# Optimization experiments

Measured on AMD Instinct MI355X. Metric: run time of the kernel, lower is better.

The kernel has to match this reference:

```python
import jax, jax.numpy as jnp
import numpy as np

EPS = 1e-5
GROUPS = 32


def group_norm(x, w, b):
    # x: [N, C]; GroupNorm over 1x1 spatial == per-group norm over C//GROUPS chans
    N, C = x.shape
    xg = x.reshape(N, GROUPS, C // GROUPS)
    mu = xg.mean(-1, keepdims=True)
    var = xg.var(-1, keepdims=True)
    xn = ((xg - mu) * jax.lax.rsqrt(var + EPS)).reshape(N, C)
    return xn * w + b


def rb(x, gn1w, gn1b, c1w, c1b, gn2w, gn2b, c2w, c2b):
    # Conv2d 3x3 pad=1 on a 1x1 spatial input: only the center tap sees data
    # (all other taps hit zero padding), so it reduces exactly to a GEMM with
    # the [out, in] center slice of the kernel.
    h = jax.nn.silu(group_norm(x, gn1w, gn1b))
    h = h @ c1w[:, :, 1, 1].T + c1b
    h = jax.nn.silu(group_norm(h, gn2w, gn2b))
    h = h @ c2w[:, :, 1, 1].T + c2b
    return h + x  # skip == Identity (in_ch == out_ch)


def setup_inputs() -> dict:
    key = jax.random.key(0)
    ks = jax.random.split(key, 20)
    BS, CAND, D, H, W = 32, 2048, 256, 32, 32
    s = 0.05
    inp = {
        "gimage": jax.random.normal(ks[0], (BS, D, H, W), dtype=jnp.float32),
        "pts": jax.random.randint(ks[1], (BS, CAND, 1, 2), 0, 256, dtype=jnp.int32),
        # two stacked RB blocks
        "gn1_w": jnp.ones((2, D), jnp.float32),
        "gn1_b": jnp.zeros((2, D), jnp.float32),
        "conv1_w": jax.random.normal(ks[2], (2, D, D, 3, 3), jnp.float32) * s,
        "conv1_b": jnp.zeros((2, D), jnp.float32),
        "gn2_w": jnp.ones((2, D), jnp.float32),
        "gn2_b": jnp.zeros((2, D), jnp.float32),
        "conv2_w": jax.random.normal(ks[3], (2, D, D, 3, 3), jnp.float32) * s,
        "conv2_b": jnp.zeros((2, D), jnp.float32),
        # class_embed: Linear(256, 2)
        "cls_w": jax.random.normal(ks[4], (2, D), jnp.float32) * s,
        "cls_b": jnp.zeros((2,), jnp.float32),
        # bbox_embed: MLP(256, 256, 4, 3)
        "mlp_w1": jax.random.normal(ks[5], (D, D), jnp.float32) * s,
        "mlp_b1": jnp.zeros((D,), jnp.float32),
        "mlp_w2": jax.random.normal(ks[6], (D, D), jnp.float32) * s,
        "mlp_b2": jnp.zeros((D,), jnp.float32),
        "mlp_w3": jax.random.normal(ks[7], (4, D), jnp.float32) * s,
        "mlp_b3": jnp.zeros((4,), jnp.float32),
    }
    return inp


def reference(gimage, pts, gn1_w, gn1_b, conv1_w, conv1_b, gn2_w, gn2_b,
              conv2_w, conv2_b, cls_w, cls_b, mlp_w1, mlp_b1, mlp_w2, mlp_b2,
              mlp_w3, mlp_b3):
    bs, C, H, W = gimage.shape
    c = pts.shape[1]
    # patch_idx = (pts // 8)[:, :, 0, :] -> (iy, ix) per (batch, candidate)
    idx = pts[:, :, 0, :] // 8                      # [bs, c, 2]
    lin = idx[..., 0] * W + idx[..., 1]             # [bs, c] flat spatial index
    g = gimage.reshape(bs, C, H * W)
    feat = jnp.take_along_axis(g, lin[:, None, :].astype(jnp.int32), axis=2)  # [bs, C, c]
    x = feat.transpose(0, 2, 1).reshape(bs * c, C)  # [(bs c), 256]

    for i in range(2):  # convLayer = Sequential(RB, RB)
        x = rb(x, gn1_w[i], gn1_b[i], conv1_w[i], conv1_b[i],
               gn2_w[i], gn2_b[i], conv2_w[i], conv2_b[i])

    logits = x @ cls_w.T + cls_b                    # [(bs c), 2]
    h = jax.nn.relu(x @ mlp_w1.T + mlp_b1)
    h = jax.nn.relu(h @ mlp_w2.T + mlp_b2)
    boxes = jax.nn.sigmoid(h @ mlp_w3.T + mlp_b3)   # [(bs c), 4]

    pred_logits = logits.reshape(bs, c, 2)
    pred_boxes = boxes.reshape(bs, c, 4)
    return pred_logits, pred_boxes
```

## Files before the change

kernel.cpp:

```cpp
#include <hip/hip_runtime.h>


typedef __attribute__((ext_vector_type(8))) _Float16 half8;
typedef __attribute__((ext_vector_type(4))) float f32x4;

#define AS 264

#define NHALF  393216
#define OFF_WC1 0
#define OFF_WC2 131072
#define OFF_W1  262144
#define OFF_W2  327680
#define WS_NEED 1572864

__device__ __forceinline__ float sigm(float y) { return 1.f / (1.f + __expf(-y)); }

template <int CTRL>
__device__ __forceinline__ float dppadd(float v) {
  union { float f; int i; } u, r;
  u.f = v;
  r.i = __builtin_amdgcn_update_dpp(0, u.i, CTRL, 0xf, 0xf, true);
  return v + r.f;
}
#define DPP_X1 0xB1
#define DPP_X2 0x4E
#define DPP_X7 0x141
#define DPP_XF 0x140

__device__ __forceinline__ float gsum8(float v) {
  v = dppadd<DPP_X1>(v);
  v = dppadd<DPP_X2>(v);
  v = dppadd<DPP_X7>(v);
  return v;
}
__device__ __forceinline__ float gsum16(float v) {
  v = dppadd<DPP_X1>(v);
  v = dppadd<DPP_X2>(v);
  v = dppadd<DPP_X7>(v);
  v = dppadd<DPP_XF>(v);
  return v;
}

__global__ __launch_bounds__(256) void prep(const float* __restrict__ c1w,
                                            const float* __restrict__ c2w,
                                            const float* __restrict__ w1,
                                            const float* __restrict__ w2,
                                            _Float16* __restrict__ ws) {
  int i = blockIdx.x * 256 + threadIdx.x;
  {
    float v = c1w[(size_t)i * 9 + 4];
    _Float16 h = (_Float16)v;
    ws[OFF_WC1 + i] = h;
    ws[NHALF + OFF_WC1 + i] = (_Float16)(v - (float)h);
  }
  {
    float v = c2w[(size_t)i * 9 + 4];
    _Float16 h = (_Float16)v;
    ws[OFF_WC2 + i] = h;
    ws[NHALF + OFF_WC2 + i] = (_Float16)(v - (float)h);
  }
  if (i < 65536) {
    float v = w1[i];
    _Float16 h = (_Float16)v;
    ws[OFF_W1 + i] = h;
    ws[NHALF + OFF_W1 + i] = (_Float16)(v - (float)h);
    v = w2[i];
    h = (_Float16)v;
    ws[OFF_W2 + i] = h;
    ws[NHALF + OFF_W2 + i] = (_Float16)(v - (float)h);
  }
}

__device__ __forceinline__ void hl_store(_Float16* __restrict__ Ah,
                                         _Float16* __restrict__ Al,
                                         int idx, float v) {
  _Float16 h = (_Float16)v;
  Ah[idx] = h;
  Al[idx] = (_Float16)(v - (float)h);
}

struct BF { half8 h[4], l[4]; };

template <int KT>
__device__ __forceinline__ void loadB(BF& B,
    const _Float16* __restrict__ Wh, const _Float16* __restrict__ Wl,
    size_t boff) {
  #pragma unroll
  for (int nt = 0; nt < 4; nt++) {
    B.h[nt] = *(const half8*)(Wh + boff + (nt << 12) + KT * 32);
    B.l[nt] = *(const half8*)(Wl + boff + (nt << 12) + KT * 32);
  }
}

template <int KT>
__device__ __forceinline__ void computeKt(f32x4 acc[2][4],
    const _Float16* __restrict__ Ah, const _Float16* __restrict__ Al,
    int aoff, const BF& B) {
  half8 ah0 = *(const half8*)(Ah + aoff + KT * 32);
  half8 ah1 = *(const half8*)(Ah + aoff + 16 * AS + KT * 32);
  half8 al0 = *(const half8*)(Al + aoff + KT * 32);
  half8 al1 = *(const half8*)(Al + aoff + 16 * AS + KT * 32);
  #pragma unroll
  for (int nt = 0; nt < 4; nt++)
    acc[0][nt] = __builtin_amdgcn_mfma_f32_16x16x32_f16(ah0, B.h[nt], acc[0][nt], 0, 0, 0);
  #pragma unroll
  for (int nt = 0; nt < 4; nt++)
    acc[1][nt] = __builtin_amdgcn_mfma_f32_16x16x32_f16(ah1, B.h[nt], acc[1][nt], 0, 0, 0);
  #pragma unroll
  for (int nt = 0; nt < 4; nt++)
    acc[0][nt] = __builtin_amdgcn_mfma_f32_16x16x32_f16(ah0, B.l[nt], acc[0][nt], 0, 0, 0);
  #pragma unroll
  for (int nt = 0; nt < 4; nt++)
    acc[1][nt] = __builtin_amdgcn_mfma_f32_16x16x32_f16(ah1, B.l[nt], acc[1][nt], 0, 0, 0);
  #pragma unroll
  for (int nt = 0; nt < 4; nt++)
    acc[0][nt] = __builtin_amdgcn_mfma_f32_16x16x32_f16(al0, B.h[nt], acc[0][nt], 0, 0, 0);
  #pragma unroll
  for (int nt = 0; nt < 4; nt++)
    acc[1][nt] = __builtin_amdgcn_mfma_f32_16x16x32_f16(al1, B.h[nt], acc[1][nt], 0, 0, 0);
}

__device__ __forceinline__ void mfma_body(f32x4 acc[2][4], BF& B0,
    const _Float16* __restrict__ Ah, const _Float16* __restrict__ Al,
    const _Float16* __restrict__ Wh, const _Float16* __restrict__ Wl,
    int aoff, size_t boff) {
  BF B1;
  #pragma unroll
  for (int mt = 0; mt < 2; mt++)
    #pragma unroll
    for (int nt = 0; nt < 4; nt++)
      acc[mt][nt] = (f32x4){0.f, 0.f, 0.f, 0.f};
  __syncthreads();
  loadB<1>(B1, Wh, Wl, boff);
  computeKt<0>(acc, Ah, Al, aoff, B0);
  loadB<2>(B0, Wh, Wl, boff);
  computeKt<1>(acc, Ah, Al, aoff, B1);
  loadB<3>(B1, Wh, Wl, boff);
  computeKt<2>(acc, Ah, Al, aoff, B0);
  loadB<4>(B0, Wh, Wl, boff);
  computeKt<3>(acc, Ah, Al, aoff, B1);
  loadB<5>(B1, Wh, Wl, boff);
  computeKt<4>(acc, Ah, Al, aoff, B0);
  loadB<6>(B0, Wh, Wl, boff);
  computeKt<5>(acc, Ah, Al, aoff, B1);
  loadB<7>(B1, Wh, Wl, boff);
  computeKt<6>(acc, Ah, Al, aoff, B0);
  computeKt<7>(acc, Ah, Al, aoff, B1);
}

__device__ __forceinline__ void gn_x_to_A(const float x[2][4][4],
    const float* __restrict__ gnw, const float* __restrict__ gnb,
    int col, int quad, int nb,
    _Float16* __restrict__ Ah, _Float16* __restrict__ Al) {
  #pragma unroll
  for (int nt = 0; nt < 4; nt++) {
    int n = nb + (nt << 4) + col;
    float gwv = gnw[n], gbv = gnb[n];
    #pragma unroll
    for (int mt = 0; mt < 2; mt++) {
      #pragma unroll
      for (int rg = 0; rg < 4; rg++) {
        float v = x[mt][nt][rg];
        float s = gsum8(v);
        float q = gsum8(v * v);
        float mu = s * 0.125f;
        float rs = rsqrtf(q * 0.125f - mu * mu + 1e-5f);
        float y = (v - mu) * rs * gwv + gbv;
        float sv = y * sigm(y);
        hl_store(Ah, Al, ((mt << 4) + (quad << 2) + rg) * AS + n, sv);
      }
    }
  }
}

__device__ __forceinline__ void epi_gn_to_A(const f32x4 acc[2][4],
    const float* __restrict__ bias,
    const float* __restrict__ gnw, const float* __restrict__ gnb,
    int col, int quad, int nb,
    _Float16* __restrict__ Ah, _Float16* __restrict__ Al) {
  #pragma unroll
  for (int nt = 0; nt < 4; nt++) {
    int n = nb + (nt << 4) + col;
    float bv = bias[n];
    float gwv = gnw[n], gbv = gnb[n];
    #pragma unroll
    for (int mt = 0; mt < 2; mt++) {
      #pragma unroll
      for (int rg = 0; rg < 4; rg++) {
        float v = acc[mt][nt][rg] + bv;
        float s = gsum8(v);
        float q = gsum8(v * v);
        float mu = s * 0.125f;
        float rs = rsqrtf(q * 0.125f - mu * mu + 1e-5f);
        float y = (v - mu) * rs * gwv + gbv;
        float sv = y * sigm(y);
        hl_store(Ah, Al, ((mt << 4) + (quad << 2) + rg) * AS + n, sv);
      }
    }
  }
}

__device__ __forceinline__ void epi_relu_to_A(const f32x4 acc[2][4],
    const float* __restrict__ bias, int col, int quad, int nb,
    _Float16* __restrict__ Ah, _Float16* __restrict__ Al) {
  #pragma unroll
  for (int nt = 0; nt < 4; nt++) {
    int n = nb + (nt << 4) + col;
    float bv = bias[n];
    #pragma unroll
    for (int mt = 0; mt < 2; mt++)
      #pragma unroll
      for (int rg = 0; rg < 4; rg++)
        hl_store(Ah, Al, ((mt << 4) + (quad << 2) + rg) * AS + n,
                 fmaxf(acc[mt][nt][rg] + bv, 0.f));
  }
}

__global__ __launch_bounds__(256, 3) void fused_mfma(
    const float* __restrict__ gimage, const int* __restrict__ pts,
    const float* __restrict__ gn1w, const float* __restrict__ gn1b,
    const float* __restrict__ c1b,
    const float* __restrict__ gn2w, const float* __restrict__ gn2b,
    const float* __restrict__ c2b,
    const float* __restrict__ clsw, const float* __restrict__ clsb,
    const float* __restrict__ b1, const float* __restrict__ b2,
    const float* __restrict__ w3, const float* __restrict__ b3,
    const _Float16* __restrict__ ws, float* __restrict__ out) {
  __shared__ _Float16 Ah[32 * AS];
  __shared__ _Float16 Al[32 * AS];
  __shared__ float red[4][32][4];

  const int t = threadIdx.x;
  const int w = t >> 6;
  const int lane = t & 63;
  const int col = lane & 15;
  const int quad = lane >> 4;
  const int nb = w << 6;
  const int bsw = ((blockIdx.x & 7) << 8) | (blockIdx.x >> 3);
  const int row0 = bsw << 5;
  const int rbase = quad << 2;

  const int aoff = col * AS + (quad << 3);
  const size_t boff = (((size_t)(nb + col)) << 8) + (quad << 3);
  const _Float16* wsl = ws + NHALF;

  float x[2][4][4];
  {
    int lin[2][4];
    #pragma unroll
    for (int mt = 0; mt < 2; mt++)
      #pragma unroll
      for (int rg = 0; rg < 4; rg++) {
        int grow = row0 + (mt << 4) + rbase + rg;
        int p0 = pts[2 * grow], p1 = pts[2 * grow + 1];
        lin[mt][rg] = ((p0 >> 3) << 5) + (p1 >> 3);
      }
    const float* gbase = gimage + (((size_t)((row0 >> 11) << 8)) << 10);
    #pragma unroll
    for (int nt = 0; nt < 4; nt++) {
      const float* gc = gbase + (((size_t)(nb + (nt << 4) + col)) << 10);
      #pragma unroll
      for (int mt = 0; mt < 2; mt++)
        #pragma unroll
        for (int rg = 0; rg < 4; rg++)
          x[mt][nt][rg] = gc[lin[mt][rg]];
    }
  }

  f32x4 acc[2][4];
  BF B0;

  loadB<0>(B0, ws + OFF_WC1, wsl + OFF_WC1, boff);
  #pragma unroll 1
  for (int rb = 0; rb < 2; rb++) {
    gn_x_to_A(x, gn1w + (rb << 8), gn1b + (rb << 8), col, quad, nb, Ah, Al);
    mfma_body(acc, B0, Ah, Al, ws + OFF_WC1 + (rb << 16),
              wsl + OFF_WC1 + (rb << 16), aoff, boff);
    __syncthreads();
    loadB<0>(B0, ws + OFF_WC2 + (rb << 16), wsl + OFF_WC2 + (rb << 16), boff);
    epi_gn_to_A(acc, c1b + (rb << 8), gn2w + (rb << 8), gn2b + (rb << 8),
                col, quad, nb, Ah, Al);
    mfma_body(acc, B0, Ah, Al, ws + OFF_WC2 + (rb << 16),
              wsl + OFF_WC2 + (rb << 16), aoff, boff);
    __syncthreads();
    if (rb == 0)
      loadB<0>(B0, ws + OFF_WC1 + 65536, wsl + OFF_WC1 + 65536, boff);
    else
      loadB<0>(B0, ws + OFF_W1, wsl + OFF_W1, boff);
    #pragma unroll
    for (int nt = 0; nt < 4; nt++) {
      float bv = c2b[(rb << 8) + nb + (nt << 4) + col];
      #pragma unroll
      for (int mt = 0; mt < 2; mt++)
        #pragma unroll
        for (int rg = 0; rg < 4; rg++)
          x[mt][nt][rg] += acc[mt][nt][rg] + bv;
    }
  }

  #pragma unroll
  for (int nt = 0; nt < 4; nt++) {
    int n = nb + (nt << 4) + col;
    #pragma unroll
    for (int mt = 0; mt < 2; mt++)
      #pragma unroll
      for (int rg = 0; rg < 4; rg++)
        hl_store(Ah, Al, ((mt << 4) + rbase + rg) * AS + n, x[mt][nt][rg]);
  }
  {
    float pc[2][2][4];
    #pragma unroll
    for (int j = 0; j < 2; j++) {
      #pragma unroll
      for (int mt = 0; mt < 2; mt++)
        #pragma unroll
        for (int rg = 0; rg < 4; rg++)
          pc[j][mt][rg] = 0.f;
      #pragma unroll
      for (int nt = 0; nt < 4; nt++) {
        float wv = clsw[(j << 8) + nb + (nt << 4) + col];
        #pragma unroll
        for (int mt = 0; mt < 2; mt++)
          #pragma unroll
          for (int rg = 0; rg < 4; rg++)
            pc[j][mt][rg] += x[mt][nt][rg] * wv;
      }
    }
    #pragma unroll
    for (int j = 0; j < 2; j++)
      #pragma unroll
      for (int mt = 0; mt < 2; mt++)
        #pragma unroll
        for (int rg = 0; rg < 4; rg++) {
          float p = gsum16(pc[j][mt][rg]);
          if (col == 0) red[w][(mt << 4) + rbase + rg][j] = p;
        }
  }

  mfma_body(acc, B0, Ah, Al, ws + OFF_W1, wsl + OFF_W1, aoff, boff);
  if (t < 64) {
    int r = t >> 1, j = t & 1;
    out[((size_t)(row0 + r) << 1) + j] =
        clsb[j] + red[0][r][j] + red[1][r][j] + red[2][r][j] + red[3][r][j];
  }
  __syncthreads();
  loadB<0>(B0, ws + OFF_W2, wsl + OFF_W2, boff);
  epi_relu_to_A(acc, b1, col, quad, nb, Ah, Al);

  mfma_body(acc, B0, Ah, Al, ws + OFF_W2, wsl + OFF_W2, aoff, boff);
  __syncthreads();
  {
    float pb[4][2][4];
    #pragma unroll
    for (int j = 0; j < 4; j++)
      #pragma unroll
      for (int mt = 0; mt < 2; mt++)
        #pragma unroll
        for (int rg = 0; rg < 4; rg++)
          pb[j][mt][rg] = 0.f;
    #pragma unroll
    for (int nt = 0; nt < 4; nt++) {
      int n = nb + (nt << 4) + col;
      float bv = b2[n];
      float w0 = w3[n], w1v = w3[256 + n], w2v = w3[512 + n], w3v = w3[768 + n];
      #pragma unroll
      for (int mt = 0; mt < 2; mt++)
        #pragma unroll
        for (int rg = 0; rg < 4; rg++) {
          float v = fmaxf(acc[mt][nt][rg] + bv, 0.f);
          pb[0][mt][rg] += v * w0;
          pb[1][mt][rg] += v * w1v;
          pb[2][mt][rg] += v * w2v;
          pb[3][mt][rg] += v * w3v;
        }
    }
    #pragma unroll
    for (int j = 0; j < 4; j++)
      #pragma unroll
      for (int mt = 0; mt < 2; mt++)
        #pragma unroll
        for (int rg = 0; rg < 4; rg++) {
          float p = gsum16(pb[j][mt][rg]);
          if (col == 0) red[w][(mt << 4) + rbase + rg][j] = p;
        }
  }
  __syncthreads();
  if (t < 128) {
    int r = t >> 2, j = t & 3;
    float s = b3[j] + red[0][r][j] + red[1][r][j] + red[2][r][j] + red[3][r][j];
    out[131072 + ((size_t)(row0 + r) << 2) + j] = sigm(s);
  }
}

#define LS 260
template <int EPI, bool CONV>
__device__ __forceinline__ void gemm_f32(const float* __restrict__ src,
                                         const float* __restrict__ W,
                                         const float* __restrict__ bias,
                                         float* __restrict__ dst,
                                         float* __restrict__ X) {
  const int n = threadIdx.x;
  float acc[32];
  #pragma unroll
  for (int r = 0; r < 32; r++) acc[r] = 0.f;
  #pragma unroll 1
  for (int k = 0; k < 256; k += 8) {
    float w[8];
    if (CONV) {
      #pragma unroll
      for (int j = 0; j < 8; j++) w[j] = W[(size_t)((n << 8) + k + j) * 9 + 4];
    } else {
      f32x4 wa = *(const f32x4*)(W + (n << 8) + k);
      f32x4 wb = *(const f32x4*)(W + (n << 8) + k + 4);
      w[0] = wa[0]; w[1] = wa[1]; w[2] = wa[2]; w[3] = wa[3];
      w[4] = wb[0]; w[5] = wb[1]; w[6] = wb[2]; w[7] = wb[3];
    }
    #pragma unroll
    for (int r = 0; r < 32; r++) {
      const float* xr = src + r * LS + k;
      f32x4 a0 = *(const f32x4*)xr, a1 = *(const f32x4*)(xr + 4);
      acc[r] += a0[0] * w[0] + a0[1] * w[1] + a0[2] * w[2] + a0[3] * w[3]
              + a1[0] * w[4] + a1[1] * w[5] + a1[2] * w[6] + a1[3] * w[7];
    }
  }
  float bv = bias[n];
  #pragma unroll
  for (int r = 0; r < 32; r++) {
    float v = acc[r] + bv;
    if (EPI == 0) dst[r * LS + n] = v;
    else if (EPI == 1) X[r * LS + n] += v;
    else dst[r * LS + n] = fmaxf(v, 0.f);
  }
}
__device__ __forceinline__ void gn_silu32(const float* __restrict__ src,
                                          float* __restrict__ dst,
                                          const float* __restrict__ gw,
                                          const float* __restrict__ gb, int t) {
  #pragma unroll
  for (int i = 0; i < 4; i++) {
    int task = (i << 8) + t;
    int r = task >> 5, g = task & 31;
    const float* x = src + r * LS + (g << 3);
    f32x4 x0 = *(const f32x4*)x, x1 = *(const f32x4*)(x + 4);
    float xx[8] = {x0[0], x0[1], x0[2], x0[3], x1[0], x1[1], x1[2], x1[3]};
    float s = 0.f, q = 0.f;
    #pragma unroll
    for (int j = 0; j < 8; j++) { s += xx[j]; q += xx[j] * xx[j]; }
    float mu = s * 0.125f;
    float rs = rsqrtf(q * 0.125f - mu * mu + 1e-5f);
    const float* w = gw + (g << 3);
    const float* b = gb + (g << 3);
    float* d = dst + r * LS + (g << 3);
    #pragma unroll
    for (int j = 0; j < 8; j++) {
      float y = (xx[j] - mu) * rs * w[j] + b[j];
      d[j] = y * sigm(y);
    }
  }
}
__global__ __launch_bounds__(256, 1) void fused_all(
    const float* __restrict__ gimage, const int* __restrict__ pts,
    const float* __restrict__ gn1w, const float* __restrict__ gn1b,
    const float* __restrict__ c1w, const float* __restrict__ c1b,
    const float* __restrict__ gn2w, const float* __restrict__ gn2b,
    const float* __restrict__ c2w, const float* __restrict__ c2b,
    const float* __restrict__ clsw, const float* __restrict__ clsb,
    const float* __restrict__ w1, const float* __restrict__ b1,
    const float* __restrict__ w2, const float* __restrict__ b2,
    const float* __restrict__ w3, const float* __restrict__ b3,
    float* __restrict__ out) {
  __shared__ float X[32 * LS];
  __shared__ float A[32 * LS];
  __shared__ float H[32 * LS];
  const int t = threadIdx.x;
  const int row0 = blockIdx.x << 5;
  {
    int r = t >> 3;
    int c0 = (t & 7) << 5;
    int grow = row0 + r;
    int p0 = pts[2 * grow], p1 = pts[2 * grow + 1];
    int lin = ((p0 >> 3) << 5) + (p1 >> 3);
    int b = grow >> 11;
    const float* src = gimage + (((size_t)((b << 8) + c0)) << 10) + lin;
    #pragma unroll
    for (int c = 0; c < 32; c++) X[r * LS + c0 + c] = src[(size_t)c << 10];
  }
  __syncthreads();
  #pragma unroll 1
  for (int rb = 0; rb < 2; rb++) {
    gn_silu32(X, A, gn1w + (rb << 8), gn1b + (rb << 8), t);
    __syncthreads();
    gemm_f32<0, true>(A, c1w + rb * 589824, c1b + (rb << 8), H, nullptr);
    __syncthreads();
    gn_silu32(H, A, gn2w + (rb << 8), gn2b + (rb << 8), t);
    __syncthreads();
    gemm_f32<1, true>(A, c2w + rb * 589824, c2b + (rb << 8), nullptr, X);
    __syncthreads();
  }
  if (t < 64) {
    int r = t >> 1, j = t & 1;
    float s = clsb[j];
    const float* w = clsw + (j << 8);
    const float* x = X + r * LS;
    #pragma unroll 1
    for (int k = 0; k < 256; k += 4) {
      f32x4 wv = *(const f32x4*)(w + k);
      f32x4 xv = *(const f32x4*)(x + k);
      s += xv[0] * wv[0] + xv[1] * wv[1] + xv[2] * wv[2] + xv[3] * wv[3];
    }
    out[((size_t)(row0 + r) << 1) + j] = s;
  }
  gemm_f32<2, false>(X, w1, b1, H, nullptr);
  __syncthreads();
  gemm_f32<2, false>(H, w2, b2, A, nullptr);
  __syncthreads();
  if (t < 128) {
    int r = t >> 2, j = t & 3;
    float s = b3[j];
    const float* w = w3 + (j << 8);
    const float* x = A + r * LS;
    #pragma unroll 1
    for (int k = 0; k < 256; k += 4) {
      f32x4 wv = *(const f32x4*)(w + k);
      f32x4 xv = *(const f32x4*)(x + k);
      s += xv[0] * wv[0] + xv[1] * wv[1] + xv[2] * wv[2] + xv[3] * wv[3];
    }
    out[131072 + ((size_t)(row0 + r) << 2) + j] = sigm(s);
  }
}

extern "C" void kernel_launch(void* const* d_in, const int* in_sizes, int n_in,
                              void* d_out, int out_size, void* d_ws, size_t ws_size,
                              hipStream_t stream) {
  const float* gimage = (const float*)d_in[0];
  const int* pts = (const int*)d_in[1];
  const float* gn1w = (const float*)d_in[2];
  const float* gn1b = (const float*)d_in[3];
  const float* c1w = (const float*)d_in[4];
  const float* c1b = (const float*)d_in[5];
  const float* gn2w = (const float*)d_in[6];
  const float* gn2b = (const float*)d_in[7];
  const float* c2w = (const float*)d_in[8];
  const float* c2b = (const float*)d_in[9];
  const float* clsw = (const float*)d_in[10];
  const float* clsb = (const float*)d_in[11];
  const float* w1 = (const float*)d_in[12];
  const float* b1 = (const float*)d_in[13];
  const float* w2 = (const float*)d_in[14];
  const float* b2 = (const float*)d_in[15];
  const float* w3 = (const float*)d_in[16];
  const float* b3 = (const float*)d_in[17];

  if (ws_size >= (size_t)WS_NEED) {
    _Float16* ws = (_Float16*)d_ws;
    prep<<<512, 256, 0, stream>>>(c1w, c2w, w1, w2, ws);
    fused_mfma<<<2048, 256, 0, stream>>>(gimage, pts, gn1w, gn1b, c1b,
                                         gn2w, gn2b, c2b, clsw, clsb,
                                         b1, b2, w3, b3, ws, (float*)d_out);
  } else {
    fused_all<<<2048, 256, 0, stream>>>(gimage, pts, gn1w, gn1b, c1w, c1b,
                                        gn2w, gn2b, c2w, c2b, clsw, clsb,
                                        w1, b1, w2, b2, w3, b3, (float*)d_out);
  }
}
```

Before: 539.0 us.

## Double-buffer LDS activation tiles to remove block barriers between GEMM stages

Splits the shared-memory A tiles into two ping-pong buffers, so that consecutive GEMM stages alternate buffers. This lets the explicit __syncthreads between each GEMM and the next epilogue write be dropped. The launch bound is lowered from 3 to 2 blocks per CU, which gives the compiler more registers per thread but may reduce occupancy. Shared memory use roughly doubles, and correctness now relies on the barriers inside mfma_body to order buffer reuse.

```diff
diff --git a/kernel.cpp b/kernel.cpp
--- a/kernel.cpp
+++ b/kernel.cpp
@@ -216,7 +216,7 @@
   }
 }
 
-__global__ __launch_bounds__(256, 3) void fused_mfma(
+__global__ __launch_bounds__(256, 2) void fused_mfma(
     const float* __restrict__ gimage, const int* __restrict__ pts,
     const float* __restrict__ gn1w, const float* __restrict__ gn1b,
     const float* __restrict__ c1b,
@@ -226,8 +226,8 @@
     const float* __restrict__ b1, const float* __restrict__ b2,
     const float* __restrict__ w3, const float* __restrict__ b3,
     const _Float16* __restrict__ ws, float* __restrict__ out) {
-  __shared__ _Float16 Ah[32 * AS];
-  __shared__ _Float16 Al[32 * AS];
+  __shared__ _Float16 Ah[2][32 * AS];
+  __shared__ _Float16 Al[2][32 * AS];
   __shared__ float red[4][32][4];
 
   const int t = threadIdx.x;
@@ -268,25 +268,24 @@
   }
 
   f32x4 acc[2][4];
-  BF B0;
-
-  loadB<0>(B0, ws + OFF_WC1, wsl + OFF_WC1, boff);
+  BF B;
+
+  loadB<0>(B, ws + OFF_WC1, wsl + OFF_WC1, boff);
   #pragma unroll 1
   for (int rb = 0; rb < 2; rb++) {
-    gn_x_to_A(x, gn1w + (rb << 8), gn1b + (rb << 8), col, quad, nb, Ah, Al);
-    mfma_body(acc, B0, Ah, Al, ws + OFF_WC1 + (rb << 16),
+    gn_x_to_A(x, gn1w + (rb << 8), gn1b + (rb << 8), col, quad, nb,
+              Ah[0], Al[0]);
+    mfma_body(acc, B, Ah[0], Al[0], ws + OFF_WC1 + (rb << 16),
               wsl + OFF_WC1 + (rb << 16), aoff, boff);
-    __syncthreads();
-    loadB<0>(B0, ws + OFF_WC2 + (rb << 16), wsl + OFF_WC2 + (rb << 16), boff);
+    loadB<0>(B, ws + OFF_WC2 + (rb << 16), wsl + OFF_WC2 + (rb << 16), boff);
     epi_gn_to_A(acc, c1b + (rb << 8), gn2w + (rb << 8), gn2b + (rb << 8),
-                col, quad, nb, Ah, Al);
-    mfma_body(acc, B0, Ah, Al, ws + OFF_WC2 + (rb << 16),
+                col, quad, nb, Ah[1], Al[1]);
+    mfma_body(acc, B, Ah[1], Al[1], ws + OFF_WC2 + (rb << 16),
               wsl + OFF_WC2 + (rb << 16), aoff, boff);
-    __syncthreads();
     if (rb == 0)
-      loadB<0>(B0, ws + OFF_WC1 + 65536, wsl + OFF_WC1 + 65536, boff);
+      loadB<0>(B, ws + OFF_WC1 + 65536, wsl + OFF_WC1 + 65536, boff);
     else
-      loadB<0>(B0, ws + OFF_W1, wsl + OFF_W1, boff);
+      loadB<0>(B, ws + OFF_W1, wsl + OFF_W1, boff);
     #pragma unroll
     for (int nt = 0; nt < 4; nt++) {
       float bv = c2b[(rb << 8) + nb + (nt << 4) + col];
@@ -305,7 +304,8 @@
     for (int mt = 0; mt < 2; mt++)
       #pragma unroll
       for (int rg = 0; rg < 4; rg++)
-        hl_store(Ah, Al, ((mt << 4) + rbase + rg) * AS + n, x[mt][nt][rg]);
+        hl_store(Ah[0], Al[0], ((mt << 4) + rbase + rg) * AS + n,
+                 x[mt][nt][rg]);
   }
   {
     float pc[2][2][4];
@@ -337,18 +337,16 @@
         }
   }
 
-  mfma_body(acc, B0, Ah, Al, ws + OFF_W1, wsl + OFF_W1, aoff, boff);
+  mfma_body(acc, B, Ah[0], Al[0], ws + OFF_W1, wsl + OFF_W1, aoff, boff);
   if (t < 64) {
     int r = t >> 1, j = t & 1;
     out[((size_t)(row0 + r) << 1) + j] =
         clsb[j] + red[0][r][j] + red[1][r][j] + red[2][r][j] + red[3][r][j];
   }
-  __syncthreads();
-  loadB<0>(B0, ws + OFF_W2, wsl + OFF_W2, boff);
-  epi_relu_to_A(acc, b1, col, quad, nb, Ah, Al);
-
-  mfma_body(acc, B0, Ah, Al, ws + OFF_W2, wsl + OFF_W2, aoff, boff);
-  __syncthreads();
+  loadB<0>(B, ws + OFF_W2, wsl + OFF_W2, boff);
+  epi_relu_to_A(acc, b1, col, quad, nb, Ah[1], Al[1]);
+
+  mfma_body(acc, B, Ah[1], Al[1], ws + OFF_W2, wsl + OFF_W2, aoff, boff);
   {
     float pb[4][2][4];
     #pragma unroll
```

Result: no change. 535.9 us (-0.6%).
